# Performance work log

Hardware: AMD Instinct MI355X
Metric: run time of the kernel (lower is better)

Reference implementation:

```python
import jax, jax.numpy as jnp
import numpy as np

B, S, M, E, DFF = 4, 2048, 1024, 8, 4096
CAPACITY_FACTOR = 1.25


def setup_inputs() -> dict:
    key = jax.random.key(0)
    k = jax.random.split(key, 5)
    x = jax.random.normal(k[0], (B, S, M), dtype=jnp.float32)
    wg = jax.random.normal(k[1], (M, E), dtype=jnp.float32) * 0.02
    w1 = jax.random.normal(k[2], (E, M, DFF), dtype=jnp.float32) * 0.02
    b1 = jnp.zeros((E, DFF), dtype=jnp.float32)
    w2 = jax.random.normal(k[3], (E, DFF, M), dtype=jnp.float32) * 0.02
    b2 = jnp.zeros((E, M), dtype=jnp.float32)
    return {"x": x, "wg": wg, "w1": w1, "b1": b1, "w2": w2, "b2": b2}


def _top1_gate(tokens, wg, capacity):
    # tokens: [T, M] -> combine_weights [T, E, C], dispatch_mask [T, E, C]
    gates = jax.nn.softmax(tokens @ wg)                      # [T, E]
    expert_idx = jnp.argmax(gates, axis=-1)                  # [T]
    mask1 = jax.nn.one_hot(expert_idx, gates.shape[-1], dtype=gates.dtype)  # [T, E]
    # position of each token within its chosen expert's queue
    pos = jnp.sum(jnp.cumsum(mask1, axis=0) * mask1, axis=-1).astype(jnp.int32) - 1  # [T]
    keep = (pos < capacity).astype(gates.dtype)              # capacity drop
    mask1c = mask1 * keep[:, None]                           # [T, E]
    gates1 = jnp.sum(gates * mask1c, axis=-1)                # chosen prob (0 if dropped)
    loc_oh = jax.nn.one_hot(pos, capacity, dtype=gates.dtype)  # [T, C] (>=C rows -> all 0)
    combine = gates1[:, None, None] * mask1c[:, :, None] * loc_oh[:, None, :]  # [T, E, C]
    dispatch = (combine > 0).astype(tokens.dtype)
    return combine, dispatch


def reference(x, wg, w1, b1, w2, b2):
    d_model = x.shape[-1]
    tokens = x.reshape(-1, d_model)                          # [T, M]
    T = tokens.shape[0]
    num_experts = wg.shape[1]
    capacity = int(CAPACITY_FACTOR * T / num_experts)        # C
    combine, dispatch = _top1_gate(tokens, wg, capacity)
    # dispatch tokens to per-expert buffers: [E, C, M]
    dispatched = jnp.einsum('sec,sm->ecm', dispatch, tokens)
    # per-expert FFN (batched over experts)
    h = jax.nn.relu(jnp.einsum('ecm,emf->ecf', dispatched, w1) + b1[:, None, :])
    expert_out = jnp.einsum('ecf,efm->ecm', h, w2) + b2[:, None, :]
    # combine back to tokens
    combined = jnp.einsum('sec,ecm->sm', combine, expert_out)
    return combined.reshape(x.shape)
```

## Files before the change

kernel.cpp:

```cpp
#include <hip/hip_runtime.h>

#define T_TOKENS 8192
#define MDIM 1024
#define NEXP 8
#define DFF_DIM 4096
#define CAP 1280

typedef __attribute__((ext_vector_type(8))) short short8;
typedef __attribute__((ext_vector_type(4))) float f32x4;

__device__ inline unsigned short f2bf(float f) {
  unsigned u = __float_as_uint(f);
  u = u + 0x7fffu + ((u >> 16) & 1u);
  return (unsigned short)(u >> 16);
}

__device__ __forceinline__ void async_ld16(const void* g, void* l) {
  __builtin_amdgcn_global_load_lds(
      (__attribute__((address_space(1))) void*)const_cast<void*>(g),
      (__attribute__((address_space(3))) void*)l, 16, 0, 0);
}

__global__ __launch_bounds__(64) void gate_kernel(const float* __restrict__ x,
    const float* __restrict__ wg, int* __restrict__ eidx, float* __restrict__ gate)
{
  const int t = blockIdx.x;
  const int lane = threadIdx.x;
  const float* xr = x + (size_t)t * MDIM;
  double acc[NEXP];
  #pragma unroll
  for (int e = 0; e < NEXP; ++e) acc[e] = 0.0;
  for (int m = lane; m < MDIM; m += 64) {
    double xv = (double)xr[m];
    const float* wr = wg + (size_t)m * NEXP;
    #pragma unroll
    for (int e = 0; e < NEXP; ++e) acc[e] += xv * (double)wr[e];
  }
  #pragma unroll
  for (int off = 32; off > 0; off >>= 1) {
    #pragma unroll
    for (int e = 0; e < NEXP; ++e) acc[e] += __shfl_down(acc[e], off);
  }
  if (lane == 0) {
    double mx = acc[0]; int idx = 0;
    #pragma unroll
    for (int e = 1; e < NEXP; ++e) if (acc[e] > mx) { mx = acc[e]; idx = e; }
    double s = 0.0;
    #pragma unroll
    for (int e = 0; e < NEXP; ++e) s += exp(acc[e] - mx);
    eidx[t] = idx;
    gate[t] = (float)(1.0 / s);
  }
}

__global__ __launch_bounds__(1024) void scan_kernel(const int* __restrict__ eidx,
    int* __restrict__ slot_token, int* __restrict__ filled)
{
  __shared__ int hist[16][NEXP];
  __shared__ int wpre[16][NEXP];
  __shared__ int rtot[NEXP];
  __shared__ int base[NEXP];
  const int tid = threadIdx.x;
  const int w = tid >> 6, lane = tid & 63;
  for (int i = tid; i < NEXP * CAP; i += 1024) slot_token[i] = -1;
  if (tid < NEXP) base[tid] = 0;
  __syncthreads();
  const unsigned long long lt = (1ull << lane) - 1ull;
  for (int r = 0; r < T_TOKENS / 1024; ++r) {
    const int t = r * 1024 + tid;
    const int e = eidx[t];
    unsigned long long bal[NEXP];
    #pragma unroll
    for (int ee = 0; ee < NEXP; ++ee) bal[ee] = __ballot(e == ee);
    const int rank = __popcll(bal[e] & lt);
    if (lane < NEXP) hist[w][lane] = __popcll(bal[lane]);
    __syncthreads();
    if (tid < 16 * NEXP) {
      int ww = tid >> 3, ee = tid & 7, s = 0;
      for (int j = 0; j < ww; ++j) s += hist[j][ee];
      wpre[ww][ee] = s;
    }
    if (tid < NEXP) {
      int s = 0;
      for (int j = 0; j < 16; ++j) s += hist[j][tid];
      rtot[tid] = s;
    }
    __syncthreads();
    const int pos = base[e] + wpre[w][e] + rank;
    if (pos < CAP) slot_token[e * CAP + pos] = t;
    __syncthreads();
    if (tid < NEXP) base[tid] += rtot[tid];
    __syncthreads();
  }
  if (tid < NEXP) filled[tid] = (base[tid] < CAP) ? base[tid] : CAP;
}

__global__ __launch_bounds__(256) void dispatch_kernel(const float* __restrict__ x,
    const int* __restrict__ slot_token, unsigned short* __restrict__ Abuf)
{
  const int row = blockIdx.x;
  const int tid = threadIdx.x;
  const int t = slot_token[row];
  unsigned short* dst = Abuf + (size_t)row * MDIM + tid * 4;
  if (t < 0) {
    ushort4 z; z.x = 0; z.y = 0; z.z = 0; z.w = 0;
    *(ushort4*)dst = z;
  } else {
    const float4 v = *(const float4*)(x + (size_t)t * MDIM + tid * 4);
    ushort4 h;
    h.x = f2bf(v.x); h.y = f2bf(v.y); h.z = f2bf(v.z); h.w = f2bf(v.w);
    *(ushort4*)dst = h;
  }
}

template<int R, int Cc>
__global__ __launch_bounds__(256) void transpose_cvt_kernel(
    const float* __restrict__ src, unsigned short* __restrict__ dst)
{
  __shared__ unsigned short tile[64][66];
  const int e = blockIdx.z;
  const int r0 = blockIdx.y * 64;
  const int c0 = blockIdx.x * 64;
  const int t = threadIdx.x;
  const float* S = src + (size_t)e * R * Cc;
  unsigned short* D = dst + (size_t)e * R * Cc;
  const int tr = t >> 4;
  const int tc = (t & 15) * 4;
  #pragma unroll
  for (int i = 0; i < 4; ++i) {
    const int row = i * 16 + tr;
    const float4 v = *(const float4*)(S + (size_t)(r0 + row) * Cc + c0 + tc);
    tile[row][tc + 0] = f2bf(v.x);
    tile[row][tc + 1] = f2bf(v.y);
    tile[row][tc + 2] = f2bf(v.z);
    tile[row][tc + 3] = f2bf(v.w);
  }
  __syncthreads();
  #pragma unroll
  for (int i = 0; i < 4; ++i) {
    const int crow = i * 16 + tr;
    ushort4 o;
    o.x = tile[tc + 0][crow];
    o.y = tile[tc + 1][crow];
    o.z = tile[tc + 2][crow];
    o.w = tile[tc + 3][crow];
    *(ushort4*)(D + (size_t)(c0 + crow) * R + r0 + tc) = o;
  }
}

template<int MODE>
__global__ __launch_bounds__(256) void gemm_kernel(
    const unsigned short* __restrict__ A, const unsigned short* __restrict__ Bt,
    const float* __restrict__ bias, void* __restrict__ outp,
    const int* __restrict__ slot_token, const float* __restrict__ gate,
    const int* __restrict__ filled)
{
  constexpr int N = MODE ? MDIM : DFF_DIM;
  constexpr int K = MODE ? DFF_DIM : MDIM;
  const int e = blockIdx.z;
  const int rowbase = blockIdx.y * 128;
  const int colbase = blockIdx.x * 128;
  if (rowbase >= filled[e]) return;

  __shared__ unsigned short As[128 * 32];
  __shared__ unsigned short Bs[128 * 32];

  const int tid = threadIdx.x;
  const int lane = tid & 63;
  const int wid = tid >> 6;
  const int wm = (wid >> 1) * 64, wn = (wid & 1) * 64;
  const int qm = lane & 15, qk = (lane >> 4) * 8, qr = lane >> 4;

  const unsigned short* Ab = A + ((size_t)e * CAP + rowbase) * K;
  const unsigned short* Bb = Bt + ((size_t)e * N + colbase) * K;

  const int ldr = wid * 16 + (lane >> 2);
  const int ldk = (lane & 3) * 8;
  const unsigned short* ag = Ab + (size_t)ldr * K + ldk;
  const unsigned short* bg = Bb + (size_t)ldr * K + ldk;
  unsigned short* asw = As + wid * 512;
  unsigned short* bsw = Bs + wid * 512;

  f32x4 acc[4][4];
  #pragma unroll
  for (int i = 0; i < 4; ++i)
    #pragma unroll
    for (int j = 0; j < 4; ++j)
      #pragma unroll
      for (int r = 0; r < 4; ++r) acc[i][j][r] = 0.0f;

  for (int k0 = 0; k0 < K; k0 += 32) {
    __syncthreads();
    async_ld16(ag + k0,                asw);
    async_ld16(ag + (size_t)64 * K + k0, asw + 2048);
    async_ld16(bg + k0,                bsw);
    async_ld16(bg + (size_t)64 * K + k0, bsw + 2048);
    __syncthreads();
    short8 af[4], bfr[4];
    #pragma unroll
    for (int i = 0; i < 4; ++i) af[i] = *(const short8*)(As + (wm + i * 16 + qm) * 32 + qk);
    #pragma unroll
    for (int j = 0; j < 4; ++j) bfr[j] = *(const short8*)(Bs + (wn + j * 16 + qm) * 32 + qk);
    #pragma unroll
    for (int i = 0; i < 4; ++i)
      #pragma unroll
      for (int j = 0; j < 4; ++j)
        acc[i][j] = __builtin_amdgcn_mfma_f32_16x16x32_bf16(af[i], bfr[j], acc[i][j], 0, 0, 0);
  }

  float bcol[4];
  #pragma unroll
  for (int j = 0; j < 4; ++j)
    bcol[j] = bias[(size_t)e * N + colbase + wn + j * 16 + qm];

  if (MODE == 0) {
    unsigned short* Hp = (unsigned short*)outp;
    #pragma unroll
    for (int i = 0; i < 4; ++i) {
      #pragma unroll
      for (int r = 0; r < 4; ++r) {
        const int row = rowbase + wm + i * 16 + qr * 4 + r;
        unsigned short* orow = Hp + ((size_t)e * CAP + row) * N + colbase;
        #pragma unroll
        for (int j = 0; j < 4; ++j) {
          float v = acc[i][j][r] + bcol[j];
          v = v > 0.0f ? v : 0.0f;
          orow[wn + j * 16 + qm] = f2bf(v);
        }
      }
    }
  } else {
    float* Op = (float*)outp;
    #pragma unroll
    for (int i = 0; i < 4; ++i) {
      #pragma unroll
      for (int r = 0; r < 4; ++r) {
        const int row = rowbase + wm + i * 16 + qr * 4 + r;
        const int t = slot_token[e * CAP + row];
        if (t >= 0) {
          const float g = gate[t];
          float* orow = Op + (size_t)t * MDIM + colbase;
          #pragma unroll
          for (int j = 0; j < 4; ++j)
            orow[wn + j * 16 + qm] = g * (acc[i][j][r] + bcol[j]);
        }
      }
    }
  }
}

extern "C" void kernel_launch(void* const* d_in, const int* in_sizes, int n_in,
                              void* d_out, int out_size, void* d_ws, size_t ws_size,
                              hipStream_t stream) {
  const float* x  = (const float*)d_in[0];
  const float* wg = (const float*)d_in[1];
  const float* w1 = (const float*)d_in[2];
  const float* b1 = (const float*)d_in[3];
  const float* w2 = (const float*)d_in[4];
  const float* b2 = (const float*)d_in[5];

  char* ws = (char*)d_ws;
  unsigned short* Abuf = (unsigned short*)ws;
  unsigned short* H    = (unsigned short*)(ws + 20971520);
  unsigned short* Wt   = (unsigned short*)(ws + 104857600);
  int*   slot_token    = (int*)(ws + 171966464);
  int*   eidx          = (int*)(ws + 172007424);
  float* gate          = (float*)(ws + 172040192);
  int*   filled        = (int*)(ws + 172072960);

  hipMemsetAsync(d_out, 0, (size_t)out_size * sizeof(float), stream);

  gate_kernel<<<T_TOKENS, 64, 0, stream>>>(x, wg, eidx, gate);
  scan_kernel<<<1, 1024, 0, stream>>>(eidx, slot_token, filled);
  dispatch_kernel<<<NEXP * CAP, 256, 0, stream>>>(x, slot_token, Abuf);

  dim3 gc1(DFF_DIM / 64, MDIM / 64, NEXP);
  transpose_cvt_kernel<MDIM, DFF_DIM><<<gc1, 256, 0, stream>>>(w1, Wt);

  dim3 g1(DFF_DIM / 128, CAP / 128, NEXP);
  gemm_kernel<0><<<g1, 256, 0, stream>>>(Abuf, Wt, b1, (void*)H, nullptr, nullptr, filled);

  dim3 gc2(MDIM / 64, DFF_DIM / 64, NEXP);
  transpose_cvt_kernel<DFF_DIM, MDIM><<<gc2, 256, 0, stream>>>(w2, Wt);

  dim3 g2(MDIM / 128, CAP / 128, NEXP);
  gemm_kernel<1><<<g2, 256, 0, stream>>>(H, Wt, b2, d_out, slot_token, gate, filled);
}
```

Before: 581.8 us.

## Double-buffer GEMM LDS tiles and remap block IDs for XCD-aware scheduling

The expert GEMM kernel now uses two LDS buffers, so the async global-to-LDS load of the next K-slice is issued before the MFMA compute on the current slice, halving the barriers per K step. The launch grid is flattened to 1D and the block id is remapped so that consecutive groups of 8 blocks (one per XCD under round-robin dispatch) are spread across column/expert tiles, with row tiles varying slowest. This aims to hide global load latency and change cache locality across chiplets, at the cost of doubled LDS use per block, which may reduce occupancy.

```diff
diff --git a/kernel.cpp b/kernel.cpp
--- a/kernel.cpp
+++ b/kernel.cpp
@@ -157,13 +157,20 @@
 {
   constexpr int N = MODE ? MDIM : DFF_DIM;
   constexpr int K = MODE ? DFF_DIM : MDIM;
-  const int e = blockIdx.z;
-  const int rowbase = blockIdx.y * 128;
-  const int colbase = blockIdx.x * 128;
+  constexpr int NCOL = N / 128;
+  constexpr int NG = NCOL * NEXP;
+  constexpr int GS = NG / 8;
+
+  const int id = blockIdx.x;
+  const int y = (id >> 3) / GS;
+  const int g = (id & 7) + 8 * ((id >> 3) % GS);
+  const int e = g / NCOL;
+  const int rowbase = y * 128;
+  const int colbase = (g % NCOL) * 128;
   if (rowbase >= filled[e]) return;
 
-  __shared__ unsigned short As[128 * 32];
-  __shared__ unsigned short Bs[128 * 32];
+  __shared__ unsigned short As[2][128 * 32];
+  __shared__ unsigned short Bs[2][128 * 32];
 
   const int tid = threadIdx.x;
   const int lane = tid & 63;
@@ -178,8 +185,7 @@
   const int ldk = (lane & 3) * 8;
   const unsigned short* ag = Ab + (size_t)ldr * K + ldk;
   const unsigned short* bg = Bb + (size_t)ldr * K + ldk;
-  unsigned short* asw = As + wid * 512;
-  unsigned short* bsw = Bs + wid * 512;
+  const int lb = wid * 512;
 
   f32x4 acc[4][4];
   #pragma unroll
@@ -189,23 +195,35 @@
       #pragma unroll
       for (int r = 0; r < 4; ++r) acc[i][j][r] = 0.0f;
 
-  for (int k0 = 0; k0 < K; k0 += 32) {
-    __syncthreads();
-    async_ld16(ag + k0,                asw);
-    async_ld16(ag + (size_t)64 * K + k0, asw + 2048);
-    async_ld16(bg + k0,                bsw);
-    async_ld16(bg + (size_t)64 * K + k0, bsw + 2048);
-    __syncthreads();
+  auto stage = [&](int k0, int buf) {
+    async_ld16(ag + k0,                  &As[buf][lb]);
+    async_ld16(ag + (size_t)64 * K + k0, &As[buf][lb + 2048]);
+    async_ld16(bg + k0,                  &Bs[buf][lb]);
+    async_ld16(bg + (size_t)64 * K + k0, &Bs[buf][lb + 2048]);
+  };
+  auto compute = [&](int buf) {
     short8 af[4], bfr[4];
     #pragma unroll
-    for (int i = 0; i < 4; ++i) af[i] = *(const short8*)(As + (wm + i * 16 + qm) * 32 + qk);
-    #pragma unroll
-    for (int j = 0; j < 4; ++j) bfr[j] = *(const short8*)(Bs + (wn + j * 16 + qm) * 32 + qk);
+    for (int i = 0; i < 4; ++i)
+      af[i] = *(const short8*)&As[buf][(wm + i * 16 + qm) * 32 + qk];
+    #pragma unroll
+    for (int j = 0; j < 4; ++j)
+      bfr[j] = *(const short8*)&Bs[buf][(wn + j * 16 + qm) * 32 + qk];
     #pragma unroll
     for (int i = 0; i < 4; ++i)
       #pragma unroll
       for (int j = 0; j < 4; ++j)
         acc[i][j] = __builtin_amdgcn_mfma_f32_16x16x32_bf16(af[i], bfr[j], acc[i][j], 0, 0, 0);
+  };
+
+  stage(0, 0);
+  for (int k0 = 0; k0 < K; k0 += 64) {
+    __syncthreads();
+    if (k0 + 32 < K) stage(k0 + 32, 1);
+    compute(0);
+    __syncthreads();
+    if (k0 + 64 < K) stage(k0 + 64, 0);
+    compute(1);
   }
 
   float bcol[4];
@@ -238,11 +256,11 @@
         const int row = rowbase + wm + i * 16 + qr * 4 + r;
         const int t = slot_token[e * CAP + row];
         if (t >= 0) {
-          const float g = gate[t];
+          const float g2 = gate[t];
           float* orow = Op + (size_t)t * MDIM + colbase;
           #pragma unroll
           for (int j = 0; j < 4; ++j)
-            orow[wn + j * 16 + qm] = g * (acc[i][j][r] + bcol[j]);
+            orow[wn + j * 16 + qm] = g2 * (acc[i][j][r] + bcol[j]);
         }
       }
     }
@@ -277,12 +295,12 @@
   dim3 gc1(DFF_DIM / 64, MDIM / 64, NEXP);
   transpose_cvt_kernel<MDIM, DFF_DIM><<<gc1, 256, 0, stream>>>(w1, Wt);
 
-  dim3 g1(DFF_DIM / 128, CAP / 128, NEXP);
-  gemm_kernel<0><<<g1, 256, 0, stream>>>(Abuf, Wt, b1, (void*)H, nullptr, nullptr, filled);
+  gemm_kernel<0><<<dim3((DFF_DIM / 128) * (CAP / 128) * NEXP), 256, 0, stream>>>(
+      Abuf, Wt, b1, (void*)H, nullptr, nullptr, filled);
 
   dim3 gc2(MDIM / 64, DFF_DIM / 64, NEXP);
   transpose_cvt_kernel<DFF_DIM, MDIM><<<gc2, 256, 0, stream>>>(w2, Wt);
 
-  dim3 g2(MDIM / 128, CAP / 128, NEXP);
-  gemm_kernel<1><<<g2, 256, 0, stream>>>(H, Wt, b2, d_out, slot_token, gate, filled);
-}
+  gemm_kernel<1><<<dim3((MDIM / 128) * (CAP / 128) * NEXP), 256, 0, stream>>>(
+      H, Wt, b2, d_out, slot_token, gate, filled);
+}
```

After: 615.5 us. 5.8% more time.
